# Kernel optimization log

Hardware: AMD Instinct MI355X
Metric: run time of the kernel (lower is better)

The kernel has to match this reference:

```python
import jax, jax.numpy as jnp
import numpy as np

N_NODES = 100000


def gcn_conv(x, W, b, src, dst, num_nodes):
    # PyG GCNConv: add self-loops, symmetric normalization, x @ W, scatter-add, + b
    xw = x @ W  # [N, out]
    loop = jnp.arange(num_nodes, dtype=src.dtype)
    s = jnp.concatenate([src, loop])  # message source j
    d = jnp.concatenate([dst, loop])  # aggregation target i
    deg = jax.ops.segment_sum(jnp.ones_like(d, dtype=xw.dtype), d, num_segments=num_nodes)
    dis = jnp.where(deg > 0, jax.lax.rsqrt(deg), 0.0)  # D^{-1/2}
    norm = dis[s] * dis[d]  # [E+N]
    msg = norm[:, None] * xw[s]  # gather + scale
    out = jax.ops.segment_sum(msg, d, num_segments=num_nodes)  # scatter-add
    return out + b


def setup_inputs() -> dict:
    key = jax.random.key(0)
    k1, k2, k3, k4 = jax.random.split(key, 4)
    F, H, E = 64, 64, 1250000
    x = jax.random.normal(k1, (N_NODES, F), dtype=jnp.float32)
    edge_index = jax.random.randint(k2, (2, E), 0, N_NODES, dtype=jnp.int64)
    W1 = jax.random.normal(k3, (F, H), dtype=jnp.float32) * (1.0 / np.sqrt(F))
    b1 = jnp.zeros((H,), dtype=jnp.float32)
    W2 = jax.random.normal(k4, (H, F), dtype=jnp.float32) * (1.0 / np.sqrt(H))
    b2 = jnp.zeros((F,), dtype=jnp.float32)
    return {"x": x, "edge_index": edge_index, "W1": W1, "b1": b1, "W2": W2, "b2": b2}


def reference(x, edge_index, W1, b1, W2, b2):
    src, dst = edge_index[0], edge_index[1]
    h = gcn_conv(x, W1, b1, src, dst, N_NODES)
    h = jax.nn.relu(h)
    out = gcn_conv(h, W2, b2, src, dst, N_NODES)
    return out
```

## Files before the change

kernel.cpp:

```cpp
#include <hip/hip_runtime.h>

#define NN    100000
#define F     64
#define NBUCK 391
#define CAPB  4096
#define TILE  4096

#define O_CURSOR 0
#define O_ROWPTR 512
#define O_DEG    100864
#define O_DIS    201216
#define O_PACKED 301568
#define O_SRT    1903104
#define O_AH     3504768
#define O_HH     6704768

__device__ __forceinline__ unsigned bf_rne(float x) {
    unsigned u = __float_as_uint(x);
    return (u + 0x7FFFu + ((u >> 16) & 1u)) >> 16;
}
__device__ __forceinline__ unsigned pack2(float lo, float hi) {
    return bf_rne(lo) | (bf_rne(hi) << 16);
}
__device__ __forceinline__ float lo_f(unsigned u) { return __uint_as_float(u << 16); }
__device__ __forceinline__ float hi_f(unsigned u) { return __uint_as_float(u & 0xFFFF0000u); }

struct BpSmem {
    int hist[NBUCK], lofs[NBUCK], gbase[NBUCK], lcur[NBUCK];
    int wsum[8];
    unsigned stage[TILE];
    unsigned short sbuck[TILE];
};
union KSmem {
    BpSmem bp;
    float wl[64 * 64];
};

__device__ __forceinline__ void binpack_body(const int* __restrict__ src,
                                             const int* __restrict__ dst, int E,
                                             int* __restrict__ cursor,
                                             unsigned* __restrict__ packed,
                                             int bid, BpSmem& sm) {
    int t  = threadIdx.x;
    int t0 = bid * TILE;
    int n  = min(TILE, E - t0);

    if (t < NBUCK) sm.hist[t] = 0;
    __syncthreads();
    for (int i = t; i < n; i += 512) atomicAdd(&sm.hist[dst[t0 + i] >> 8], 1);
    __syncthreads();
    int lane = t & 63, w = t >> 6;
    int v = (t < NBUCK) ? sm.hist[t] : 0;
    int s = v;
#pragma unroll
    for (int off = 1; off < 64; off <<= 1) {
        int u = __shfl_up(s, off, 64);
        if (lane >= off) s += u;
    }
    if (lane == 63) sm.wsum[w] = s;
    __syncthreads();
    if (t == 0) {
        int run = 0;
#pragma unroll
        for (int i = 0; i < 8; ++i) { int c = sm.wsum[i]; sm.wsum[i] = run; run += c; }
    }
    __syncthreads();
    if (t < NBUCK) {
        int ex = s - v + sm.wsum[w];
        sm.lofs[t] = ex;
        sm.lcur[t] = ex;
        sm.gbase[t] = t * CAPB + (v ? atomicAdd(&cursor[t], v) : 0);
    }
    __syncthreads();
    for (int i = t; i < n; i += 512) {
        int d = dst[t0 + i];
        int b = d >> 8;
        int p = atomicAdd(&sm.lcur[b], 1);
        sm.stage[p] = ((unsigned)src[t0 + i] << 8) | (unsigned)(d & 255);
        sm.sbuck[p] = (unsigned short)b;
    }
    __syncthreads();
    for (int i = t; i < n; i += 512) {
        int b = sm.sbuck[i];
        packed[sm.gbase[b] + (i - sm.lofs[b])] = sm.stage[i];
    }
}

__device__ __forceinline__ void gemm_body(const float* __restrict__ X,
                                          const float* __restrict__ W,
                                          unsigned* __restrict__ Ah, int bid,
                                          float* wl) {
    int t = threadIdx.x;
    for (int i = t; i < 64 * 64; i += 512) wl[i] = W[i];
    __syncthreads();
    int lane = t & 63;
    int w    = t >> 6;
    float Wreg[64];
#pragma unroll
    for (int k = 0; k < 64; ++k) Wreg[k] = wl[k * 64 + lane];

    int row0 = bid * 32 + w * 4;
    const float* xp = X + (size_t)row0 * F;
    float xa = xp[lane];
    float xb = xp[64 + lane];
    float xc = xp[128 + lane];
    float xd = xp[192 + lane];
    float a0 = 0.f, a1 = 0.f, a2 = 0.f, a3 = 0.f;
#pragma unroll
    for (int k = 0; k < 64; ++k) {
        float wv = Wreg[k];
        a0 = fmaf(__uint_as_float(__builtin_amdgcn_readlane(__float_as_uint(xa), k)), wv, a0);
        a1 = fmaf(__uint_as_float(__builtin_amdgcn_readlane(__float_as_uint(xb), k)), wv, a1);
        a2 = fmaf(__uint_as_float(__builtin_amdgcn_readlane(__float_as_uint(xc), k)), wv, a2);
        a3 = fmaf(__uint_as_float(__builtin_amdgcn_readlane(__float_as_uint(xd), k)), wv, a3);
    }
    float p0 = __shfl_xor(a0, 1, 64);
    float p1 = __shfl_xor(a1, 1, 64);
    float p2 = __shfl_xor(a2, 1, 64);
    float p3 = __shfl_xor(a3, 1, 64);
    if (!(lane & 1)) {
        int c = lane >> 1;
        Ah[(size_t)(row0 + 0) * 32 + c] = pack2(a0, p0);
        Ah[(size_t)(row0 + 1) * 32 + c] = pack2(a1, p1);
        Ah[(size_t)(row0 + 2) * 32 + c] = pack2(a2, p2);
        Ah[(size_t)(row0 + 3) * 32 + c] = pack2(a3, p3);
    }
}

__device__ __forceinline__ void gemm_h_body(const unsigned* __restrict__ Hh,
                                            const float* __restrict__ W,
                                            unsigned* __restrict__ Ah, int bid,
                                            float* wl) {
    int t = threadIdx.x;
    for (int i = t; i < 64 * 64; i += 512) wl[i] = W[i];
    __syncthreads();
    int lane = t & 63;
    int w    = t >> 6;
    float Wreg[64];
#pragma unroll
    for (int k = 0; k < 64; ++k) Wreg[k] = wl[k * 64 + lane];

    int row0 = bid * 32 + w * 4;
    int l = lane & 31, r = lane >> 5;
    unsigned pa = Hh[(size_t)(row0 + r) * 32 + l];
    unsigned pb = Hh[(size_t)(row0 + 2 + r) * 32 + l];
    float a0 = 0.f, a1 = 0.f, a2 = 0.f, a3 = 0.f;
#pragma unroll
    for (int k = 0; k < 64; ++k) {
        float wv = Wreg[k];
        unsigned q0 = __builtin_amdgcn_readlane(pa, k >> 1);
        unsigned q1 = __builtin_amdgcn_readlane(pa, 32 + (k >> 1));
        unsigned q2 = __builtin_amdgcn_readlane(pb, k >> 1);
        unsigned q3 = __builtin_amdgcn_readlane(pb, 32 + (k >> 1));
        float x0 = (k & 1) ? hi_f(q0) : lo_f(q0);
        float x1 = (k & 1) ? hi_f(q1) : lo_f(q1);
        float x2 = (k & 1) ? hi_f(q2) : lo_f(q2);
        float x3 = (k & 1) ? hi_f(q3) : lo_f(q3);
        a0 = fmaf(x0, wv, a0);
        a1 = fmaf(x1, wv, a1);
        a2 = fmaf(x2, wv, a2);
        a3 = fmaf(x3, wv, a3);
    }
    float p0 = __shfl_xor(a0, 1, 64);
    float p1 = __shfl_xor(a1, 1, 64);
    float p2 = __shfl_xor(a2, 1, 64);
    float p3 = __shfl_xor(a3, 1, 64);
    if (!(lane & 1)) {
        int c = lane >> 1;
        Ah[(size_t)(row0 + 0) * 32 + c] = pack2(a0, p0);
        Ah[(size_t)(row0 + 1) * 32 + c] = pack2(a1, p1);
        Ah[(size_t)(row0 + 2) * 32 + c] = pack2(a2, p2);
        Ah[(size_t)(row0 + 3) * 32 + c] = pack2(a3, p3);
    }
}

__global__ __launch_bounds__(512) void pre_gemm1(const int* __restrict__ src,
                                                 const int* __restrict__ dst, int E,
                                                 int nbp, int* __restrict__ cursor,
                                                 unsigned* __restrict__ packed,
                                                 const float* __restrict__ X,
                                                 const float* __restrict__ W1,
                                                 unsigned* __restrict__ Ah) {
    __shared__ KSmem sm;
    if ((int)blockIdx.x < nbp)
        binpack_body(src, dst, E, cursor, packed, blockIdx.x, sm.bp);
    else
        gemm_body(X, W1, Ah, blockIdx.x - nbp, sm.wl);
}

__global__ __launch_bounds__(512) void gemm2h(const unsigned* __restrict__ Hh,
                                              const float* __restrict__ W,
                                              unsigned* __restrict__ Ah) {
    __shared__ float wl[64 * 64];
    gemm_h_body(Hh, W, Ah, blockIdx.x, wl);
}

__global__ __launch_bounds__(512) void node_sort(const unsigned* __restrict__ packed,
                                                 const int* __restrict__ cursor,
                                                 int* __restrict__ row_ptr,
                                                 int* __restrict__ deg,
                                                 float* __restrict__ dis,
                                                 int* __restrict__ srt) {
    __shared__ int h[256];
    __shared__ int lcur[256];
    __shared__ int wsum[4];
    __shared__ int stage[CAPB];
    int b = blockIdx.x, t = threadIdx.x;
    int nbase = b << 8;
    int nloc = min(256, NN - nbase);
    int beg = b * CAPB;
    int n = cursor[b];

    if (t < 256) h[t] = 0;
    __syncthreads();
    for (int i = t; i < n; i += 512)
        atomicAdd(&h[packed[beg + i] & 255u], 1);
    __syncthreads();
    int lane = t & 63, w = t >> 6;
    int v = 0, s = 0;
    if (t < 256) { v = h[t]; s = v; }
#pragma unroll
    for (int off = 1; off < 64; off <<= 1) {
        int u = __shfl_up(s, off, 64);
        if (lane >= off) s += u;
    }
    if (t < 256 && lane == 63) wsum[w] = s;
    __syncthreads();
    if (t == 0) {
        int run = 0;
#pragma unroll
        for (int i = 0; i < 4; ++i) { int c = wsum[i]; wsum[i] = run; run += c; }
    }
    __syncthreads();
    if (t < 256) {
        int e0 = s - v + wsum[w];
        lcur[t] = e0;
        if (t < nloc) {
            row_ptr[nbase + t] = beg + e0;
            deg[nbase + t]     = v;
            dis[nbase + t]     = rsqrtf((float)v + 1.0f);
        }
    }
    __syncthreads();
    for (int i = t; i < n; i += 512) {
        unsigned p = packed[beg + i];
        int pos = atomicAdd(&lcur[p & 255u], 1);
        stage[pos] = (int)(p >> 8);
    }
    __syncthreads();
    for (int i = t; i < n; i += 512) srt[beg + i] = stage[i];
}

template <int MODE>
__global__ __launch_bounds__(256) void agg_out(const uint2* __restrict__ Ah2,
                                               const int* __restrict__ row_ptr,
                                               const int* __restrict__ deg,
                                               const int* __restrict__ srt,
                                               const float* __restrict__ dis,
                                               const float* __restrict__ bias,
                                               void* __restrict__ outp) {
    int sub  = threadIdx.x & 15;
    int node = blockIdx.x * 16 + (threadIdx.x >> 4);
    int beg = row_ptr[node];
    int end = beg + deg[node];
    float di = dis[node];
    uint2 su = Ah2[(size_t)node * 16 + sub];
    float4 acc;
    acc.x = di * lo_f(su.x);
    acc.y = di * hi_f(su.x);
    acc.z = di * lo_f(su.y);
    acc.w = di * hi_f(su.y);
    int j = beg;
    for (; j + 4 <= end; j += 4) {
        int s0 = srt[j], s1 = srt[j + 1], s2 = srt[j + 2], s3 = srt[j + 3];
        float d0 = dis[s0], d1 = dis[s1], d2 = dis[s2], d3 = dis[s3];
        uint2 g0 = Ah2[(size_t)s0 * 16 + sub];
        uint2 g1 = Ah2[(size_t)s1 * 16 + sub];
        uint2 g2 = Ah2[(size_t)s2 * 16 + sub];
        uint2 g3 = Ah2[(size_t)s3 * 16 + sub];
        acc.x = fmaf(d0, lo_f(g0.x), fmaf(d1, lo_f(g1.x), fmaf(d2, lo_f(g2.x), fmaf(d3, lo_f(g3.x), acc.x))));
        acc.y = fmaf(d0, hi_f(g0.x), fmaf(d1, hi_f(g1.x), fmaf(d2, hi_f(g2.x), fmaf(d3, hi_f(g3.x), acc.y))));
        acc.z = fmaf(d0, lo_f(g0.y), fmaf(d1, lo_f(g1.y), fmaf(d2, lo_f(g2.y), fmaf(d3, lo_f(g3.y), acc.z))));
        acc.w = fmaf(d0, hi_f(g0.y), fmaf(d1, hi_f(g1.y), fmaf(d2, hi_f(g2.y), fmaf(d3, hi_f(g3.y), acc.w))));
    }
    for (; j < end; ++j) {
        int s0 = srt[j];
        float d0 = dis[s0];
        uint2 g0 = Ah2[(size_t)s0 * 16 + sub];
        acc.x = fmaf(d0, lo_f(g0.x), acc.x);
        acc.y = fmaf(d0, hi_f(g0.x), acc.y);
        acc.z = fmaf(d0, lo_f(g0.y), acc.z);
        acc.w = fmaf(d0, hi_f(g0.y), acc.w);
    }
    float4 bb = ((const float4*)bias)[sub];
    float4 o;
    o.x = fmaf(di, acc.x, bb.x);
    o.y = fmaf(di, acc.y, bb.y);
    o.z = fmaf(di, acc.z, bb.z);
    o.w = fmaf(di, acc.w, bb.w);
    if (MODE == 1) {
        o.x = fmaxf(o.x, 0.f); o.y = fmaxf(o.y, 0.f);
        o.z = fmaxf(o.z, 0.f); o.w = fmaxf(o.w, 0.f);
        uint2 pk;
        pk.x = pack2(o.x, o.y);
        pk.y = pack2(o.z, o.w);
        ((uint2*)outp)[(size_t)node * 16 + sub] = pk;
    } else {
        ((float4*)outp)[(size_t)node * 16 + sub] = o;
    }
}

extern "C" void kernel_launch(void* const* d_in, const int* in_sizes, int n_in,
                              void* d_out, int out_size, void* d_ws, size_t ws_size,
                              hipStream_t stream) {
    const float* x  = (const float*)d_in[0];
    const int*   ei = (const int*)d_in[1];
    const float* W1 = (const float*)d_in[2];
    const float* b1 = (const float*)d_in[3];
    const float* W2 = (const float*)d_in[4];
    const float* b2 = (const float*)d_in[5];
    float* out = (float*)d_out;
    int E = in_sizes[1] / 2;
    const int* src = ei;
    const int* dst = ei + E;

    int*      ws_i    = (int*)d_ws;
    int*      cursor  = ws_i + O_CURSOR;
    int*      row_ptr = ws_i + O_ROWPTR;
    int*      deg     = ws_i + O_DEG;
    float*    dis     = (float*)(ws_i + O_DIS);
    unsigned* packed  = (unsigned*)(ws_i + O_PACKED);
    int*      srt     = ws_i + O_SRT;
    unsigned* Ah      = (unsigned*)(ws_i + O_AH);
    unsigned* Hh      = (unsigned*)(ws_i + O_HH);

    int nbp = (E + TILE - 1) / TILE;

    hipMemsetAsync(cursor, 0, NBUCK * sizeof(int), stream);
    pre_gemm1<<<nbp + NN / 32, 512, 0, stream>>>(src, dst, E, nbp, cursor, packed,
                                                 x, W1, Ah);
    node_sort<<<NBUCK, 512, 0, stream>>>(packed, cursor, row_ptr, deg, dis, srt);
    agg_out<1><<<NN / 16, 256, 0, stream>>>((const uint2*)Ah, row_ptr, deg, srt,
                                            dis, b1, Hh);
    gemm2h<<<NN / 32, 512, 0, stream>>>(Hh, W2, Ah);
    agg_out<0><<<NN / 16, 256, 0, stream>>>((const uint2*)Ah, row_ptr, deg, srt,
                                            dis, b2, out);
}
```

Measured before the change: 210.0 us.

## Fuse layer-1 aggregation with second GEMM and split GEMM1 across sort kernel

The layer-1 aggregation kernel now computes the second linear transform in place. Each wave broadcasts its freshly aggregated bf16 rows with readlane and multiplies them by W2 staged in shared memory, so the intermediate H buffer and the separate gemm2 launch are gone. The first GEMM's blocks are also split: part runs alongside edge binning and the rest alongside the node sort, which balances the two kernels and removes one launch. The cost is an extra W2 load into LDS for every 16-node aggregation block, plus more register and LDS pressure in the gather kernel, which may lower its occupancy.

```diff
diff --git a/kernel.cpp b/kernel.cpp
--- a/kernel.cpp
+++ b/kernel.cpp
@@ -5,6 +5,8 @@
 #define NBUCK 391
 #define CAPB  4096
 #define TILE  4096
+#define G1A   1600
+#define G1TOT 3125
 
 #define O_CURSOR 0
 #define O_ROWPTR 512
@@ -13,7 +15,7 @@
 #define O_PACKED 301568
 #define O_SRT    1903104
 #define O_AH     3504768
-#define O_HH     6704768
+#define O_BH     6704768
 
 __device__ __forceinline__ unsigned bf_rne(float x) {
     unsigned u = __float_as_uint(x);
@@ -35,6 +37,14 @@
     BpSmem bp;
     float wl[64 * 64];
 };
+struct NsSmem {
+    int h[256], lcur[256], wsum[4];
+    int stage[CAPB];
+};
+union K2Smem {
+    NsSmem ns;
+    float wl[64 * 64];
+};
 
 __device__ __forceinline__ void binpack_body(const int* __restrict__ src,
                                              const int* __restrict__ dst, int E,
@@ -127,51 +137,57 @@
     }
 }
 
-__device__ __forceinline__ void gemm_h_body(const unsigned* __restrict__ Hh,
-                                            const float* __restrict__ W,
-                                            unsigned* __restrict__ Ah, int bid,
-                                            float* wl) {
+__device__ __forceinline__ void node_sort_body(const unsigned* __restrict__ packed,
+                                               const int* __restrict__ cursor,
+                                               int* __restrict__ row_ptr,
+                                               int* __restrict__ deg,
+                                               float* __restrict__ dis,
+                                               int* __restrict__ srt,
+                                               int b, NsSmem& sm) {
     int t = threadIdx.x;
-    for (int i = t; i < 64 * 64; i += 512) wl[i] = W[i];
-    __syncthreads();
-    int lane = t & 63;
-    int w    = t >> 6;
-    float Wreg[64];
-#pragma unroll
-    for (int k = 0; k < 64; ++k) Wreg[k] = wl[k * 64 + lane];
-
-    int row0 = bid * 32 + w * 4;
-    int l = lane & 31, r = lane >> 5;
-    unsigned pa = Hh[(size_t)(row0 + r) * 32 + l];
-    unsigned pb = Hh[(size_t)(row0 + 2 + r) * 32 + l];
-    float a0 = 0.f, a1 = 0.f, a2 = 0.f, a3 = 0.f;
-#pragma unroll
-    for (int k = 0; k < 64; ++k) {
-        float wv = Wreg[k];
-        unsigned q0 = __builtin_amdgcn_readlane(pa, k >> 1);
-        unsigned q1 = __builtin_amdgcn_readlane(pa, 32 + (k >> 1));
-        unsigned q2 = __builtin_amdgcn_readlane(pb, k >> 1);
-        unsigned q3 = __builtin_amdgcn_readlane(pb, 32 + (k >> 1));
-        float x0 = (k & 1) ? hi_f(q0) : lo_f(q0);
-        float x1 = (k & 1) ? hi_f(q1) : lo_f(q1);
-        float x2 = (k & 1) ? hi_f(q2) : lo_f(q2);
-        float x3 = (k & 1) ? hi_f(q3) : lo_f(q3);
-        a0 = fmaf(x0, wv, a0);
-        a1 = fmaf(x1, wv, a1);
-        a2 = fmaf(x2, wv, a2);
-        a3 = fmaf(x3, wv, a3);
-    }
-    float p0 = __shfl_xor(a0, 1, 64);
-    float p1 = __shfl_xor(a1, 1, 64);
-    float p2 = __shfl_xor(a2, 1, 64);
-    float p3 = __shfl_xor(a3, 1, 64);
-    if (!(lane & 1)) {
-        int c = lane >> 1;
-        Ah[(size_t)(row0 + 0) * 32 + c] = pack2(a0, p0);
-        Ah[(size_t)(row0 + 1) * 32 + c] = pack2(a1, p1);
-        Ah[(size_t)(row0 + 2) * 32 + c] = pack2(a2, p2);
-        Ah[(size_t)(row0 + 3) * 32 + c] = pack2(a3, p3);
-    }
+    int nbase = b << 8;
+    int nloc = min(256, NN - nbase);
+    int beg = b * CAPB;
+    int n = cursor[b];
+
+    if (t < 256) sm.h[t] = 0;
+    __syncthreads();
+    for (int i = t; i < n; i += 512)
+        atomicAdd(&sm.h[packed[beg + i] & 255u], 1);
+    __syncthreads();
+    int lane = t & 63, w = t >> 6;
+    int v = 0, s = 0;
+    if (t < 256) { v = sm.h[t]; s = v; }
+#pragma unroll
+    for (int off = 1; off < 64; off <<= 1) {
+        int u = __shfl_up(s, off, 64);
+        if (lane >= off) s += u;
+    }
+    if (t < 256 && lane == 63) sm.wsum[w] = s;
+    __syncthreads();
+    if (t == 0) {
+        int run = 0;
+#pragma unroll
+        for (int i = 0; i < 4; ++i) { int c = sm.wsum[i]; sm.wsum[i] = run; run += c; }
+    }
+    __syncthreads();
+    if (t < 256) {
+        int e0 = s - v + sm.wsum[w];
+        sm.lcur[t] = e0;
+        if (t < nloc) {
+            row_ptr[nbase + t] = beg + e0;
+            deg[nbase + t]     = v;
+            dis[nbase + t]     = rsqrtf((float)v + 1.0f);
+        }
+    }
+    __syncthreads();
+    for (int i = t; i < n; i += 512) {
+        unsigned p = packed[beg + i];
+        int pos = atomicAdd(&sm.lcur[p & 255u], 1);
+        sm.stage[pos] = (int)(p >> 8);
+    }
+    __syncthreads();
+    for (int i = t; i < n; i += 512) srt[beg + i] = sm.stage[i];
 }
 
 __global__ __launch_bounds__(512) void pre_gemm1(const int* __restrict__ src,
@@ -185,80 +201,126 @@
     if ((int)blockIdx.x < nbp)
         binpack_body(src, dst, E, cursor, packed, blockIdx.x, sm.bp);
     else
-        gemm_body(X, W1, Ah, blockIdx.x - nbp, sm.wl);
-}
-
-__global__ __launch_bounds__(512) void gemm2h(const unsigned* __restrict__ Hh,
-                                              const float* __restrict__ W,
-                                              unsigned* __restrict__ Ah) {
+        gemm_body(X, W1, Ah, (int)blockIdx.x - nbp, sm.wl);
+}
+
+__global__ __launch_bounds__(512) void sort_gemm1(const unsigned* __restrict__ packed,
+                                                  const int* __restrict__ cursor,
+                                                  int* __restrict__ row_ptr,
+                                                  int* __restrict__ deg,
+                                                  float* __restrict__ dis,
+                                                  int* __restrict__ srt,
+                                                  const float* __restrict__ X,
+                                                  const float* __restrict__ W1,
+                                                  unsigned* __restrict__ Ah) {
+    __shared__ K2Smem sm;
+    if ((int)blockIdx.x < NBUCK)
+        node_sort_body(packed, cursor, row_ptr, deg, dis, srt, blockIdx.x, sm.ns);
+    else
+        gemm_body(X, W1, Ah, G1A + (int)blockIdx.x - NBUCK, sm.wl);
+}
+
+__global__ __launch_bounds__(256) void agg1_gemm2(const uint2* __restrict__ Ah2,
+                                                  const int* __restrict__ row_ptr,
+                                                  const int* __restrict__ deg,
+                                                  const int* __restrict__ srt,
+                                                  const float* __restrict__ dis,
+                                                  const float* __restrict__ b1,
+                                                  const float* __restrict__ W2,
+                                                  unsigned* __restrict__ Bh) {
     __shared__ float wl[64 * 64];
-    gemm_h_body(Hh, W, Ah, blockIdx.x, wl);
-}
-
-__global__ __launch_bounds__(512) void node_sort(const unsigned* __restrict__ packed,
-                                                 const int* __restrict__ cursor,
-                                                 int* __restrict__ row_ptr,
-                                                 int* __restrict__ deg,
-                                                 float* __restrict__ dis,
-                                                 int* __restrict__ srt) {
-    __shared__ int h[256];
-    __shared__ int lcur[256];
-    __shared__ int wsum[4];
-    __shared__ int stage[CAPB];
-    int b = blockIdx.x, t = threadIdx.x;
-    int nbase = b << 8;
-    int nloc = min(256, NN - nbase);
-    int beg = b * CAPB;
-    int n = cursor[b];
-
-    if (t < 256) h[t] = 0;
-    __syncthreads();
-    for (int i = t; i < n; i += 512)
-        atomicAdd(&h[packed[beg + i] & 255u], 1);
-    __syncthreads();
-    int lane = t & 63, w = t >> 6;
-    int v = 0, s = 0;
-    if (t < 256) { v = h[t]; s = v; }
-#pragma unroll
-    for (int off = 1; off < 64; off <<= 1) {
-        int u = __shfl_up(s, off, 64);
-        if (lane >= off) s += u;
-    }
-    if (t < 256 && lane == 63) wsum[w] = s;
-    __syncthreads();
-    if (t == 0) {
-        int run = 0;
-#pragma unroll
-        for (int i = 0; i < 4; ++i) { int c = wsum[i]; wsum[i] = run; run += c; }
-    }
-    __syncthreads();
-    if (t < 256) {
-        int e0 = s - v + wsum[w];
-        lcur[t] = e0;
-        if (t < nloc) {
-            row_ptr[nbase + t] = beg + e0;
-            deg[nbase + t]     = v;
-            dis[nbase + t]     = rsqrtf((float)v + 1.0f);
-        }
-    }
-    __syncthreads();
-    for (int i = t; i < n; i += 512) {
-        unsigned p = packed[beg + i];
-        int pos = atomicAdd(&lcur[p & 255u], 1);
-        stage[pos] = (int)(p >> 8);
-    }
-    __syncthreads();
-    for (int i = t; i < n; i += 512) srt[beg + i] = stage[i];
-}
-
-template <int MODE>
+    int t = threadIdx.x;
+    for (int i = t; i < 64 * 64; i += 256) wl[i] = W2[i];
+    __syncthreads();
+
+    int sub  = t & 15;
+    int node = blockIdx.x * 16 + (t >> 4);
+    int beg = row_ptr[node];
+    int end = beg + deg[node];
+    float di = dis[node];
+    uint2 su = Ah2[(size_t)node * 16 + sub];
+    float4 acc;
+    acc.x = di * lo_f(su.x);
+    acc.y = di * hi_f(su.x);
+    acc.z = di * lo_f(su.y);
+    acc.w = di * hi_f(su.y);
+    int j = beg;
+    for (; j + 4 <= end; j += 4) {
+        int s0 = srt[j], s1 = srt[j + 1], s2 = srt[j + 2], s3 = srt[j + 3];
+        float d0 = dis[s0], d1 = dis[s1], d2 = dis[s2], d3 = dis[s3];
+        uint2 g0 = Ah2[(size_t)s0 * 16 + sub];
+        uint2 g1 = Ah2[(size_t)s1 * 16 + sub];
+        uint2 g2 = Ah2[(size_t)s2 * 16 + sub];
+        uint2 g3 = Ah2[(size_t)s3 * 16 + sub];
+        acc.x = fmaf(d0, lo_f(g0.x), fmaf(d1, lo_f(g1.x), fmaf(d2, lo_f(g2.x), fmaf(d3, lo_f(g3.x), acc.x))));
+        acc.y = fmaf(d0, hi_f(g0.x), fmaf(d1, hi_f(g1.x), fmaf(d2, hi_f(g2.x), fmaf(d3, hi_f(g3.x), acc.y))));
+        acc.z = fmaf(d0, lo_f(g0.y), fmaf(d1, lo_f(g1.y), fmaf(d2, lo_f(g2.y), fmaf(d3, lo_f(g3.y), acc.z))));
+        acc.w = fmaf(d0, hi_f(g0.y), fmaf(d1, hi_f(g1.y), fmaf(d2, hi_f(g2.y), fmaf(d3, hi_f(g3.y), acc.w))));
+    }
+    for (; j < end; ++j) {
+        int s0 = srt[j];
+        float d0 = dis[s0];
+        uint2 g0 = Ah2[(size_t)s0 * 16 + sub];
+        acc.x = fmaf(d0, lo_f(g0.x), acc.x);
+        acc.y = fmaf(d0, hi_f(g0.x), acc.y);
+        acc.z = fmaf(d0, lo_f(g0.y), acc.z);
+        acc.w = fmaf(d0, hi_f(g0.y), acc.w);
+    }
+    float4 bb = ((const float4*)b1)[sub];
+    float4 o;
+    o.x = fmaxf(fmaf(di, acc.x, bb.x), 0.f);
+    o.y = fmaxf(fmaf(di, acc.y, bb.y), 0.f);
+    o.z = fmaxf(fmaf(di, acc.z, bb.z), 0.f);
+    o.w = fmaxf(fmaf(di, acc.w, bb.w), 0.f);
+    unsigned pkx = pack2(o.x, o.y);
+    unsigned pky = pack2(o.z, o.w);
+
+    int lane = t & 63;
+    float a0 = 0.f, a1 = 0.f, a2 = 0.f, a3 = 0.f;
+#pragma unroll
+    for (int kq = 0; kq < 16; ++kq) {
+        float w0 = wl[(4 * kq + 0) * 64 + lane];
+        float w1 = wl[(4 * kq + 1) * 64 + lane];
+        float w2 = wl[(4 * kq + 2) * 64 + lane];
+        float w3 = wl[(4 * kq + 3) * 64 + lane];
+        unsigned qx0 = __builtin_amdgcn_readlane(pkx, kq);
+        unsigned qy0 = __builtin_amdgcn_readlane(pky, kq);
+        unsigned qx1 = __builtin_amdgcn_readlane(pkx, 16 + kq);
+        unsigned qy1 = __builtin_amdgcn_readlane(pky, 16 + kq);
+        unsigned qx2 = __builtin_amdgcn_readlane(pkx, 32 + kq);
+        unsigned qy2 = __builtin_amdgcn_readlane(pky, 32 + kq);
+        unsigned qx3 = __builtin_amdgcn_readlane(pkx, 48 + kq);
+        unsigned qy3 = __builtin_amdgcn_readlane(pky, 48 + kq);
+        a0 = fmaf(lo_f(qx0), w0, a0); a0 = fmaf(hi_f(qx0), w1, a0);
+        a0 = fmaf(lo_f(qy0), w2, a0); a0 = fmaf(hi_f(qy0), w3, a0);
+        a1 = fmaf(lo_f(qx1), w0, a1); a1 = fmaf(hi_f(qx1), w1, a1);
+        a1 = fmaf(lo_f(qy1), w2, a1); a1 = fmaf(hi_f(qy1), w3, a1);
+        a2 = fmaf(lo_f(qx2), w0, a2); a2 = fmaf(hi_f(qx2), w1, a2);
+        a2 = fmaf(lo_f(qy2), w2, a2); a2 = fmaf(hi_f(qy2), w3, a2);
+        a3 = fmaf(lo_f(qx3), w0, a3); a3 = fmaf(hi_f(qx3), w1, a3);
+        a3 = fmaf(lo_f(qy3), w2, a3); a3 = fmaf(hi_f(qy3), w3, a3);
+    }
+    float p0 = __shfl_xor(a0, 1, 64);
+    float p1 = __shfl_xor(a1, 1, 64);
+    float p2 = __shfl_xor(a2, 1, 64);
+    float p3 = __shfl_xor(a3, 1, 64);
+    if (!(lane & 1)) {
+        int c = lane >> 1;
+        int row0 = blockIdx.x * 16 + (t >> 6) * 4;
+        Bh[(size_t)(row0 + 0) * 32 + c] = pack2(a0, p0);
+        Bh[(size_t)(row0 + 1) * 32 + c] = pack2(a1, p1);
+        Bh[(size_t)(row0 + 2) * 32 + c] = pack2(a2, p2);
+        Bh[(size_t)(row0 + 3) * 32 + c] = pack2(a3, p3);
+    }
+}
+
 __global__ __launch_bounds__(256) void agg_out(const uint2* __restrict__ Ah2,
                                                const int* __restrict__ row_ptr,
                                                const int* __restrict__ deg,
                                                const int* __restrict__ srt,
                                                const float* __restrict__ dis,
                                                const float* __restrict__ bias,
-                                               void* __restrict__ outp) {
+                                               float* __restrict__ outp) {
     int sub  = threadIdx.x & 15;
     int node = blockIdx.x * 16 + (threadIdx.x >> 4);
     int beg = row_ptr[node];
@@ -298,16 +360,7 @@
     o.y = fmaf(di, acc.y, bb.y);
     o.z = fmaf(di, acc.z, bb.z);
     o.w = fmaf(di, acc.w, bb.w);
-    if (MODE == 1) {
-        o.x = fmaxf(o.x, 0.f); o.y = fmaxf(o.y, 0.f);
-        o.z = fmaxf(o.z, 0.f); o.w = fmaxf(o.w, 0.f);
-        uint2 pk;
-        pk.x = pack2(o.x, o.y);
-        pk.y = pack2(o.z, o.w);
-        ((uint2*)outp)[(size_t)node * 16 + sub] = pk;
-    } else {
-        ((float4*)outp)[(size_t)node * 16 + sub] = o;
-    }
+    ((float4*)outp)[(size_t)node * 16 + sub] = o;
 }
 
 extern "C" void kernel_launch(void* const* d_in, const int* in_sizes, int n_in,
@@ -332,17 +385,17 @@
     unsigned* packed  = (unsigned*)(ws_i + O_PACKED);
     int*      srt     = ws_i + O_SRT;
     unsigned* Ah      = (unsigned*)(ws_i + O_AH);
-    unsigned* Hh      = (unsigned*)(ws_i + O_HH);
+    unsigned* Bh      = (unsigned*)(ws_i + O_BH);
 
     int nbp = (E + TILE - 1) / TILE;
 
     hipMemsetAsync(cursor, 0, NBUCK * sizeof(int), stream);
-    pre_gemm1<<<nbp + NN / 32, 512, 0, stream>>>(src, dst, E, nbp, cursor, packed,
-                                                 x, W1, Ah);
-    node_sort<<<NBUCK, 512, 0, stream>>>(packed, cursor, row_ptr, deg, dis, srt);
-    agg_out<1><<<NN / 16, 256, 0, stream>>>((const uint2*)Ah, row_ptr, deg, srt,
-                                            dis, b1, Hh);
-    gemm2h<<<NN / 32, 512, 0, stream>>>(Hh, W2, Ah);
-    agg_out<0><<<NN / 16, 256, 0, stream>>>((const uint2*)Ah, row_ptr, deg, srt,
-                                            dis, b2, out);
-}
+    pre_gemm1<<<nbp + G1A, 512, 0, stream>>>(src, dst, E, nbp, cursor, packed,
+                                             x, W1, Ah);
+    sort_gemm1<<<NBUCK + (G1TOT - G1A), 512, 0, stream>>>(packed, cursor, row_ptr,
+                                                          deg, dis, srt, x, W1, Ah);
+    agg1_gemm2<<<NN / 16, 256, 0, stream>>>((const uint2*)Ah, row_ptr, deg, srt,
+                                            dis, b1, W2, Bh);
+    agg_out<<<NN / 16, 256, 0, stream>>>((const uint2*)Bh, row_ptr, deg, srt,
+                                         dis, b2, out);
+}
```

Measured after the change: 200.7 us. 1.05x faster.
